# Kernel tuning notes

Measured on AMD Instinct MI355X. Metric: run time of the kernel, lower is better.

Reference implementation:

```python
import jax, jax.numpy as jnp
import numpy as np

HEADS = 8
DIM_HEAD = 64

def setup_inputs() -> dict:
    key = jax.random.key(0)
    ks = jax.random.split(key, 5)
    B, n, dim = 128, 512, 256
    inner = HEADS * DIM_HEAD  # 512
    return {
        'x': jax.random.normal(ks[0], (B, n, dim), dtype=jnp.float32),
        'Wq': jax.random.normal(ks[1], (dim, inner), dtype=jnp.float32) * (dim ** -0.5),
        'Wkv': jax.random.normal(ks[2], (dim, 2 * inner), dtype=jnp.float32) * (dim ** -0.5),
        'Wo': jax.random.normal(ks[3], (inner, dim), dtype=jnp.float32) * (inner ** -0.5),
        'bo': jnp.zeros((dim,), dtype=jnp.float32),
        'tie_attn_dim': 64,
    }

def reference(x, Wq, Wkv, Wo, bo, tie_attn_dim):
    h, dh = HEADS, DIM_HEAD
    B, n, dim = x.shape
    r = tie_attn_dim
    b = B // r
    q = x @ Wq                      # [B, n, h*dh]
    kv = x @ Wkv                    # [B, n, 2*h*dh] (self-attention: context = x)
    k, v = jnp.split(kv, 2, axis=-1)
    # '(b r) n (h d) -> b r h n d'
    def to_tied(t):
        return t.reshape(b, r, n, h, dh).transpose(0, 1, 3, 2, 4)
    q, k, v = map(to_tied, (q, k, v))
    scale = (dh ** -0.5) * (r ** -0.5)
    # tied row attention: reduce over MSA rows r and head dim d
    dots = jnp.einsum('brhid,brhjd->bhij', q, k) * scale  # [b, h, n, n]
    attn = jax.nn.softmax(dots, axis=-1)
    out = jnp.einsum('bhij,brhjd->brhid', attn, v)        # [b, r, h, n, dh]
    # 'b r h n d -> (b r) n (h d)'
    out = out.transpose(0, 1, 3, 2, 4).reshape(B, n, h * dh)
    return out @ Wo + bo
```

## Files before the change

kernel.cpp:

```cpp
#include <hip/hip_runtime.h>

typedef unsigned short u16;
typedef __attribute__((ext_vector_type(8))) short bf16x8;
typedef __attribute__((ext_vector_type(4))) float f32x4;

struct __align__(8) U16x4 { u16 a, b, c, d; };

__device__ __forceinline__ u16 f2bf(float f) {
  union { float f; unsigned int u; } cv; cv.f = f;
  unsigned int u = cv.u;
  unsigned int r = (u + 0x7fffu + ((u >> 16) & 1u)) >> 16;
  return (u16)r;
}

__device__ __forceinline__ void gld16(const u16* g, u16* l) {
  __builtin_amdgcn_global_load_lds((const __attribute__((address_space(1))) void*)g,
                                   (__attribute__((address_space(3))) void*)l, 16, 0, 0);
}

__global__ void conv_k(const float* __restrict__ x, u16* __restrict__ xbf) {
  size_t i = ((size_t)blockIdx.x * 256 + threadIdx.x) * 8;
  u16 tmp[8];
  #pragma unroll
  for (int j = 0; j < 8; j++) tmp[j] = f2bf(x[i + j]);
  *(bf16x8*)&xbf[i] = *(const bf16x8*)&tmp[0];
}

__global__ void prep_k(const float* __restrict__ Wq, const float* __restrict__ Wkv,
                       const float* __restrict__ Wo, u16* __restrict__ WT1,
                       u16* __restrict__ WoT) {
  int idx = blockIdx.x * 256 + threadIdx.x;
  if (idx < 1536 * 256) {
    int c = idx >> 8, k = idx & 255;
    WT1[idx] = (c < 512) ? f2bf(Wq[(size_t)k * 512 + c])
                         : f2bf(Wkv[(size_t)k * 1024 + (c - 512)]);
  }
  if (idx < 256 * 512) {
    int nn = idx >> 9, kk = idx & 511;
    WoT[idx] = f2bf(Wo[(size_t)kk * 256 + nn]);
  }
}

template<int KIND>
__global__ void __launch_bounds__(256, 3) gemm_k(
    const u16* __restrict__ A, const u16* __restrict__ B,
    u16* __restrict__ C, u16* __restrict__ C2,
    float* __restrict__ SF, const float* __restrict__ bias,
    int aux0, int nk32) {
  __shared__ __align__(16) u16 lsm[16384];
  u16* lAq[2] = { lsm,        lsm + 4096 };
  u16* lBq[2] = { lsm + 8192, lsm + 12288 };

  const int tid  = threadIdx.x;
  const int bid  = blockIdx.x;
  const int lane = tid & 63;
  const int wv   = tid >> 6;
  const int l15  = lane & 15;
  const int quad = lane >> 4;
  const int mq   = (wv & 1) * 64;
  const int nq   = (wv >> 1) * 64;

  int m0, n0, NK2, kb0 = 0;
  int s = 0, p = 0;
  if constexpr (KIND == 1) {
    int nwg = aux0 * 12;
    int per = nwg >> 3;
    int sw  = (bid & 7) * per + (bid >> 3);
    m0 = (sw / 12) * 128; n0 = (sw % 12) * 128; NK2 = 4;
  } else if constexpr (KIND == 2) {
    int npS = aux0;
    n0 = (bid & 3) * 128; m0 = ((bid >> 2) & 3) * 128;
    p = (bid >> 4) & ((1 << npS) - 1); s = bid >> (4 + npS);
    NK2 = nk32 >> 1; kb0 = s * nk32;
  } else if constexpr (KIND == 3) {
    n0 = (bid & 31) * 128; m0 = ((bid >> 5) & 3) * 128; p = bid >> 7; NK2 = 8;
  } else {
    n0 = (bid & 1) * 128; m0 = (bid >> 1) * 128; NK2 = 8;
  }

  f32x4 acc[4][4];
  #pragma unroll
  for (int i = 0; i < 4; i++)
    #pragma unroll
    for (int j = 0; j < 4; j++)
      #pragma unroll
      for (int g = 0; g < 4; g++) acc[i][j][g] = 0.f;

  const int ar0 = tid >> 2;
  const int ac0 = (tid & 3) * 8;

  for (int t = 0; t < NK2; t++) {
    #pragma unroll
    for (int q = 0; q < 2; q++) {
      const int kb = kb0 + 2 * t + q;
      size_t aBase, bBase; int aRS, bRS;
      if constexpr (KIND == 1) {
        aBase = (size_t)m0 * 256 + kb * 32; aRS = 256;
        bBase = (size_t)n0 * 256 + kb * 32; bRS = 256;
      } else if constexpr (KIND == 2) {
        int bt = p >> 3, hl = p & 7;
        int r = kb >> 1, dlo = (kb & 1) * 32;
        size_t rowblk = (size_t)bt * 32768 + (size_t)r * 512;
        aBase = (rowblk + m0) * 1024 + hl * 64 + dlo;        aRS = 1024;
        bBase = (rowblk + n0) * 1024 + 512 + hl * 64 + dlo;  bRS = 1024;
      } else if constexpr (KIND == 3) {
        aBase = ((size_t)p * 512 + m0) * 512 + kb * 32;   aRS = 512;
        bBase = ((size_t)p * 4096 + n0) * 512 + kb * 32;  bRS = 512;
      } else {
        int bt = m0 >> 15, h = kb >> 1, dlo = (kb & 1) * 32;
        aBase = ((size_t)(bt * 8 + h) * 512 + (m0 & 511)) * 4096
                + ((m0 >> 9) & 63) * 64 + dlo;
        aRS = 4096;
        bBase = (size_t)n0 * 512 + kb * 32; bRS = 512;
      }
      gld16(A + aBase + (size_t)ar0 * aRS + ac0,        &lAq[q][tid * 8]);
      gld16(A + aBase + (size_t)(ar0 + 64) * aRS + ac0, &lAq[q][(tid + 256) * 8]);
      gld16(B + bBase + (size_t)ar0 * bRS + ac0,        &lBq[q][tid * 8]);
      gld16(B + bBase + (size_t)(ar0 + 64) * bRS + ac0, &lBq[q][(tid + 256) * 8]);
    }
    __syncthreads();

    #pragma unroll
    for (int q = 0; q < 2; q++) {
      bf16x8 af[4], bfr[4];
      #pragma unroll
      for (int mi = 0; mi < 4; mi++)
        af[mi] = *(const bf16x8*)&lAq[q][(mq + mi * 16 + l15) * 32 + quad * 8];
      #pragma unroll
      for (int ni = 0; ni < 4; ni++)
        bfr[ni] = *(const bf16x8*)&lBq[q][(nq + ni * 16 + l15) * 32 + quad * 8];
      #pragma unroll
      for (int mi = 0; mi < 4; mi++)
        #pragma unroll
        for (int ni = 0; ni < 4; ni++)
          acc[mi][ni] = __builtin_amdgcn_mfma_f32_16x16x32_bf16(af[mi], bfr[ni], acc[mi][ni], 0, 0, 0);
    }
    __syncthreads();
  }

  if constexpr (KIND == 1 || KIND == 3) {
    if (KIND == 3 || n0 < 1024) {
      #pragma unroll
      for (int ps = 0; ps < 2; ps++) {
        if ((mq >> 6) == ps) {
          #pragma unroll
          for (int mi = 0; mi < 4; mi++)
            #pragma unroll
            for (int ni = 0; ni < 4; ni++) {
              int lr = mi * 16 + quad * 4;
              int lc = nq + ni * 16 + l15;
              #pragma unroll
              for (int g = 0; g < 4; g++)
                lsm[(lr + g) * 136 + lc] = f2bf(acc[mi][ni][g]);
            }
        }
        __syncthreads();
        #pragma unroll
        for (int it = 0; it < 4; it++) {
          int idx = tid + it * 256;
          int lr = idx >> 4, c = (idx & 15) * 8;
          int gm = m0 + ps * 64 + lr;
          size_t gaddr;
          if constexpr (KIND == 1) gaddr = (size_t)gm * 1024 + n0 + c;
          else                     gaddr = ((size_t)p * 512 + gm) * 4096 + n0 + c;
          *(bf16x8*)&C[gaddr] = *(const bf16x8*)&lsm[lr * 136 + c];
        }
        __syncthreads();
      }
    } else {
      #pragma unroll
      for (int ps = 0; ps < 2; ps++) {
        if ((nq >> 6) == ps) {
          #pragma unroll
          for (int mi = 0; mi < 4; mi++)
            #pragma unroll
            for (int ni = 0; ni < 4; ni++) {
              int lrn = ni * 16 + l15;
              int lcm = mq + mi * 16 + quad * 4;
              U16x4 pk;
              pk.a = f2bf(acc[mi][ni][0]); pk.b = f2bf(acc[mi][ni][1]);
              pk.c = f2bf(acc[mi][ni][2]); pk.d = f2bf(acc[mi][ni][3]);
              *(U16x4*)&lsm[lrn * 136 + lcm] = pk;
            }
        }
        __syncthreads();
        int bt2 = m0 >> 15;
        int r  = (m0 >> 9) & 63;
        int jb = (m0 & 511);
        #pragma unroll
        for (int it = 0; it < 4; it++) {
          int idx = tid + it * 256;
          int lr = idx >> 4, c = (idx & 15) * 8;
          int cc = (n0 - 1024) + ps * 64 + lr;
          int h = cc >> 6, d = cc & 63;
          size_t gaddr = ((size_t)(bt2 * 8 + h) * 4096 + r * 64 + d) * 512 + jb + c;
          *(bf16x8*)&C2[gaddr] = *(const bf16x8*)&lsm[lr * 136 + c];
        }
        __syncthreads();
      }
    }
  } else {
    float* lsf = (float*)lsm;
    #pragma unroll
    for (int ps = 0; ps < 4; ps++) {
      if ((mq >> 6) == (ps >> 1)) {
        int miA = (ps & 1) * 2;
        #pragma unroll
        for (int mm = 0; mm < 2; mm++) {
          int mi = miA + mm;
          #pragma unroll
          for (int ni = 0; ni < 4; ni++) {
            int lr = mm * 16 + quad * 4;
            int lc = nq + ni * 16 + l15;
            #pragma unroll
            for (int g = 0; g < 4; g++)
              lsf[(lr + g) * 132 + lc] = acc[mi][ni][g];
          }
        }
      }
      __syncthreads();
      #pragma unroll
      for (int it = 0; it < 4; it++) {
        int idx = tid + it * 256;
        int lr = idx >> 5, c = (idx & 31) * 4;
        int gm = m0 + ps * 32 + lr;
        f32x4 v = *(const f32x4*)&lsf[lr * 132 + c];
        if constexpr (KIND == 2) {
          int npS = aux0;
          *(f32x4*)&SF[((size_t)((s << npS) + p) * 512 + gm) * 512 + n0 + c] = v;
        } else {
          f32x4 bo4 = *(const f32x4*)&bias[n0 + c];
          v[0] += bo4[0]; v[1] += bo4[1]; v[2] += bo4[2]; v[3] += bo4[3];
          *(f32x4*)&SF[(size_t)gm * 256 + n0 + c] = v;
        }
      }
      __syncthreads();
    }
  }
}

__global__ void softmax_k(const float* __restrict__ SP, u16* __restrict__ P,
                          int nsplit, int np) {
  int bid = blockIdx.x;
  int p = bid >> 9, i = bid & 511;
  int t = threadIdx.x;
  size_t rowbase = ((size_t)p * 512 + i) * 512;
  float v0 = 0.f, v1 = 0.f;
  for (int ss = 0; ss < nsplit; ss++) {
    size_t off = (size_t)ss * np * 512 * 512;
    v0 += SP[off + rowbase + t];
    v1 += SP[off + rowbase + t + 256];
  }
  const float scale = 1.0f / 64.0f;
  v0 *= scale; v1 *= scale;

  int wv = t >> 6, ln = t & 63;
  float m = fmaxf(v0, v1);
  for (int o = 32; o > 0; o >>= 1) m = fmaxf(m, __shfl_down(m, o));
  __shared__ float sred[4];
  if (ln == 0) sred[wv] = m;
  __syncthreads();
  m = fmaxf(fmaxf(sred[0], sred[1]), fmaxf(sred[2], sred[3]));

  float e0 = expf(v0 - m), e1 = expf(v1 - m);
  float sum = e0 + e1;
  for (int o = 32; o > 0; o >>= 1) sum += __shfl_down(sum, o);
  __shared__ float sred2[4];
  if (ln == 0) sred2[wv] = sum;
  __syncthreads();
  float inv = 1.0f / (sred2[0] + sred2[1] + sred2[2] + sred2[3]);

  P[rowbase + t]       = f2bf(e0 * inv);
  P[rowbase + t + 256] = f2bf(e1 * inv);
}

extern "C" void kernel_launch(void* const* d_in, const int* in_sizes, int n_in,
                              void* d_out, int out_size, void* d_ws, size_t ws_size,
                              hipStream_t stream) {
  (void)in_sizes; (void)n_in; (void)out_size;
  const float* x   = (const float*)d_in[0];
  const float* Wq  = (const float*)d_in[1];
  const float* Wkv = (const float*)d_in[2];
  const float* Wo  = (const float*)d_in[3];
  const float* bo  = (const float*)d_in[4];
  float* out = (float*)d_out;

  const size_t MB = 1024ull * 1024ull;
  int nsplit_m = (ws_size >= 266 * MB) ? 4 : 2;
  bool merged = (ws_size >= 202 * MB + ((nsplit_m * 16 * MB > 33 * MB)
                                         ? nsplit_m * 16 * MB : 33 * MB));

  char* ws = (char*)d_ws;
  size_t off = 0;
  u16* WT1 = (u16*)(ws + off); off += (size_t)1536 * 256 * 2;
  u16* WoT = (u16*)(ws + off); off += (size_t)256 * 512 * 2;

  prep_k<<<dim3(1536), dim3(256), 0, stream>>>(Wq, Wkv, Wo, WT1, WoT);

  if (merged) {
    const int np = 16, npS = 4, ns = nsplit_m;
    u16* QK = (u16*)(ws + off); off += (size_t)65536 * 1024 * 2;
    u16* OT = QK;
    u16* VT = (u16*)(ws + off); off += (size_t)np * 4096 * 512 * 2;
    u16* Pb = (u16*)(ws + off); off += (size_t)np * 512 * 512 * 2;
    char* XS = ws + off;
    u16* xbf = (u16*)XS;
    float* SP = (float*)XS;

    conv_k<<<dim3(8192), dim3(256), 0, stream>>>(x, xbf);
    gemm_k<1><<<dim3(512 * 12), dim3(256), 0, stream>>>(xbf, WT1, QK, VT,
                                                        nullptr, nullptr, 512, 0);
    gemm_k<2><<<dim3(ns * np * 16), dim3(256), 0, stream>>>(QK, QK, nullptr, nullptr,
                                                            SP, nullptr, npS, 128 / ns);
    softmax_k<<<dim3(np * 512), dim3(256), 0, stream>>>(SP, Pb, ns, np);
    gemm_k<3><<<dim3(np * 128), dim3(256), 0, stream>>>(Pb, VT, OT, nullptr,
                                                        nullptr, nullptr, 0, 0);
    gemm_k<4><<<dim3(1024), dim3(256), 0, stream>>>(OT, WoT, nullptr, nullptr,
                                                    out, bo, 0, 0);
  } else {
    const int np = 8, npS = 3;
    u16* QKb = (u16*)(ws + off); off += (size_t)32768 * 1024 * 2;
    u16* OTb = QKb;
    u16* VTb = (u16*)(ws + off); off += (size_t)np * 4096 * 512 * 2;
    u16* Pb  = (u16*)(ws + off); off += (size_t)np * 512 * 512 * 2;
    char* XS = ws + off;
    u16* xbf = (u16*)XS;
    float* SPb = (float*)XS;
    size_t rem = (ws_size > off) ? (ws_size - off) : 0;
    int ns = 4;
    while (ns > 1 && (size_t)ns * np * 512 * 512 * 4 > rem) ns >>= 1;

    for (int bt = 0; bt < 2; bt++) {
      const float* xb = x + (size_t)bt * 32768 * 256;
      float* outb = out + (size_t)bt * 32768 * 256;
      conv_k<<<dim3(4096), dim3(256), 0, stream>>>(xb, xbf);
      gemm_k<1><<<dim3(256 * 12), dim3(256), 0, stream>>>(xbf, WT1, QKb, VTb,
                                                          nullptr, nullptr, 256, 0);
      gemm_k<2><<<dim3(ns * np * 16), dim3(256), 0, stream>>>(QKb, QKb, nullptr, nullptr,
                                                              SPb, nullptr, npS, 128 / ns);
      softmax_k<<<dim3(np * 512), dim3(256), 0, stream>>>(SPb, Pb, ns, np);
      gemm_k<3><<<dim3(np * 128), dim3(256), 0, stream>>>(Pb, VTb, OTb, nullptr,
                                                          nullptr, nullptr, 0, 0);
      gemm_k<4><<<dim3(512), dim3(256), 0, stream>>>(OTb, WoT, nullptr, nullptr,
                                                     outb, bo, 0, 0);
    }
  }
}
```

Before: 358.0 us.

## Fuse fp32-to-bf16 conversion of x into projection GEMM loads

Removes the separate conv_k pass and has the QKV projection GEMM read fp32 x directly, converting to bf16 in registers before writing to LDS, which drops one full read and write of x. The softmax kernel now loads float2 and stores packed bf16 pairs, which changes the column-to-thread mapping but stays consistent. The split count for the scores GEMM is fixed at 2 and the workspace threshold for the merged path is changed. In exchange the A operand of the first GEMM loses the async global-to-LDS load and goes through registers with synchronous loads, and it needs twice the bytes per element.

```diff
diff --git a/kernel.cpp b/kernel.cpp
--- a/kernel.cpp
+++ b/kernel.cpp
@@ -16,14 +16,6 @@
 __device__ __forceinline__ void gld16(const u16* g, u16* l) {
   __builtin_amdgcn_global_load_lds((const __attribute__((address_space(1))) void*)g,
                                    (__attribute__((address_space(3))) void*)l, 16, 0, 0);
-}
-
-__global__ void conv_k(const float* __restrict__ x, u16* __restrict__ xbf) {
-  size_t i = ((size_t)blockIdx.x * 256 + threadIdx.x) * 8;
-  u16 tmp[8];
-  #pragma unroll
-  for (int j = 0; j < 8; j++) tmp[j] = f2bf(x[i + j]);
-  *(bf16x8*)&xbf[i] = *(const bf16x8*)&tmp[0];
 }
 
 __global__ void prep_k(const float* __restrict__ Wq, const float* __restrict__ Wkv,
@@ -93,30 +85,48 @@
     #pragma unroll
     for (int q = 0; q < 2; q++) {
       const int kb = kb0 + 2 * t + q;
-      size_t aBase, bBase; int aRS, bRS;
       if constexpr (KIND == 1) {
-        aBase = (size_t)m0 * 256 + kb * 32; aRS = 256;
-        bBase = (size_t)n0 * 256 + kb * 32; bRS = 256;
-      } else if constexpr (KIND == 2) {
-        int bt = p >> 3, hl = p & 7;
-        int r = kb >> 1, dlo = (kb & 1) * 32;
-        size_t rowblk = (size_t)bt * 32768 + (size_t)r * 512;
-        aBase = (rowblk + m0) * 1024 + hl * 64 + dlo;        aRS = 1024;
-        bBase = (rowblk + n0) * 1024 + 512 + hl * 64 + dlo;  bRS = 1024;
-      } else if constexpr (KIND == 3) {
-        aBase = ((size_t)p * 512 + m0) * 512 + kb * 32;   aRS = 512;
-        bBase = ((size_t)p * 4096 + n0) * 512 + kb * 32;  bRS = 512;
+        const float* xf = (const float*)A;
+        const float* pa = xf + (size_t)m0 * 256 + (size_t)kb * 32
+                             + (size_t)ar0 * 256 + ac0;
+        f32x4 u0 = *(const f32x4*)pa;
+        f32x4 u1 = *(const f32x4*)(pa + 4);
+        f32x4 u2 = *(const f32x4*)(pa + 64 * 256);
+        f32x4 u3 = *(const f32x4*)(pa + 64 * 256 + 4);
+        u16 c0[8], c1[8];
+        #pragma unroll
+        for (int j = 0; j < 4; j++) {
+          c0[j] = f2bf(u0[j]); c0[j + 4] = f2bf(u1[j]);
+          c1[j] = f2bf(u2[j]); c1[j + 4] = f2bf(u3[j]);
+        }
+        *(bf16x8*)&lAq[q][tid * 8]         = *(const bf16x8*)&c0[0];
+        *(bf16x8*)&lAq[q][(tid + 256) * 8] = *(const bf16x8*)&c1[0];
+        size_t bBase = (size_t)n0 * 256 + kb * 32;
+        gld16(B + bBase + (size_t)ar0 * 256 + ac0,        &lBq[q][tid * 8]);
+        gld16(B + bBase + (size_t)(ar0 + 64) * 256 + ac0, &lBq[q][(tid + 256) * 8]);
       } else {
-        int bt = m0 >> 15, h = kb >> 1, dlo = (kb & 1) * 32;
-        aBase = ((size_t)(bt * 8 + h) * 512 + (m0 & 511)) * 4096
-                + ((m0 >> 9) & 63) * 64 + dlo;
-        aRS = 4096;
-        bBase = (size_t)n0 * 512 + kb * 32; bRS = 512;
-      }
-      gld16(A + aBase + (size_t)ar0 * aRS + ac0,        &lAq[q][tid * 8]);
-      gld16(A + aBase + (size_t)(ar0 + 64) * aRS + ac0, &lAq[q][(tid + 256) * 8]);
-      gld16(B + bBase + (size_t)ar0 * bRS + ac0,        &lBq[q][tid * 8]);
-      gld16(B + bBase + (size_t)(ar0 + 64) * bRS + ac0, &lBq[q][(tid + 256) * 8]);
+        size_t aBase, bBase; int aRS, bRS;
+        if constexpr (KIND == 2) {
+          int bt = p >> 3, hl = p & 7;
+          int r = kb >> 1, dlo = (kb & 1) * 32;
+          size_t rowblk = (size_t)bt * 32768 + (size_t)r * 512;
+          aBase = (rowblk + m0) * 1024 + hl * 64 + dlo;        aRS = 1024;
+          bBase = (rowblk + n0) * 1024 + 512 + hl * 64 + dlo;  bRS = 1024;
+        } else if constexpr (KIND == 3) {
+          aBase = ((size_t)p * 512 + m0) * 512 + kb * 32;   aRS = 512;
+          bBase = ((size_t)p * 4096 + n0) * 512 + kb * 32;  bRS = 512;
+        } else {
+          int bt = m0 >> 15, h = kb >> 1, dlo = (kb & 1) * 32;
+          aBase = ((size_t)(bt * 8 + h) * 512 + (m0 & 511)) * 4096
+                  + ((m0 >> 9) & 63) * 64 + dlo;
+          aRS = 4096;
+          bBase = (size_t)n0 * 512 + kb * 32; bRS = 512;
+        }
+        gld16(A + aBase + (size_t)ar0 * aRS + ac0,        &lAq[q][tid * 8]);
+        gld16(A + aBase + (size_t)(ar0 + 64) * aRS + ac0, &lAq[q][(tid + 256) * 8]);
+        gld16(B + bBase + (size_t)ar0 * bRS + ac0,        &lBq[q][tid * 8]);
+        gld16(B + bBase + (size_t)(ar0 + 64) * bRS + ac0, &lBq[q][(tid + 256) * 8]);
+      }
     }
     __syncthreads();
 
@@ -248,8 +258,8 @@
   float v0 = 0.f, v1 = 0.f;
   for (int ss = 0; ss < nsplit; ss++) {
     size_t off = (size_t)ss * np * 512 * 512;
-    v0 += SP[off + rowbase + t];
-    v1 += SP[off + rowbase + t + 256];
+    float2 u = *(const float2*)&SP[off + rowbase + 2 * t];
+    v0 += u.x; v1 += u.y;
   }
   const float scale = 1.0f / 64.0f;
   v0 *= scale; v1 *= scale;
@@ -270,8 +280,9 @@
   __syncthreads();
   float inv = 1.0f / (sred2[0] + sred2[1] + sred2[2] + sred2[3]);
 
-  P[rowbase + t]       = f2bf(e0 * inv);
-  P[rowbase + t + 256] = f2bf(e1 * inv);
+  unsigned int pk = (unsigned int)f2bf(e0 * inv)
+                  | ((unsigned int)f2bf(e1 * inv) << 16);
+  *(unsigned int*)&P[rowbase + 2 * t] = pk;
 }
 
 extern "C" void kernel_launch(void* const* d_in, const int* in_sizes, int n_in,
@@ -286,9 +297,8 @@
   float* out = (float*)d_out;
 
   const size_t MB = 1024ull * 1024ull;
-  int nsplit_m = (ws_size >= 266 * MB) ? 4 : 2;
-  bool merged = (ws_size >= 202 * MB + ((nsplit_m * 16 * MB > 33 * MB)
-                                         ? nsplit_m * 16 * MB : 33 * MB));
+  const int ns_m = 2;
+  bool merged = (ws_size >= 240 * MB);
 
   char* ws = (char*)d_ws;
   size_t off = 0;
@@ -298,17 +308,14 @@
   prep_k<<<dim3(1536), dim3(256), 0, stream>>>(Wq, Wkv, Wo, WT1, WoT);
 
   if (merged) {
-    const int np = 16, npS = 4, ns = nsplit_m;
+    const int np = 16, npS = 4, ns = ns_m;
     u16* QK = (u16*)(ws + off); off += (size_t)65536 * 1024 * 2;
     u16* OT = QK;
     u16* VT = (u16*)(ws + off); off += (size_t)np * 4096 * 512 * 2;
     u16* Pb = (u16*)(ws + off); off += (size_t)np * 512 * 512 * 2;
-    char* XS = ws + off;
-    u16* xbf = (u16*)XS;
-    float* SP = (float*)XS;
-
-    conv_k<<<dim3(8192), dim3(256), 0, stream>>>(x, xbf);
-    gemm_k<1><<<dim3(512 * 12), dim3(256), 0, stream>>>(xbf, WT1, QK, VT,
+    float* SP = (float*)(ws + off);
+
+    gemm_k<1><<<dim3(512 * 12), dim3(256), 0, stream>>>((const u16*)x, WT1, QK, VT,
                                                         nullptr, nullptr, 512, 0);
     gemm_k<2><<<dim3(ns * np * 16), dim3(256), 0, stream>>>(QK, QK, nullptr, nullptr,
                                                             SP, nullptr, npS, 128 / ns);
@@ -323,18 +330,15 @@
     u16* OTb = QKb;
     u16* VTb = (u16*)(ws + off); off += (size_t)np * 4096 * 512 * 2;
     u16* Pb  = (u16*)(ws + off); off += (size_t)np * 512 * 512 * 2;
-    char* XS = ws + off;
-    u16* xbf = (u16*)XS;
-    float* SPb = (float*)XS;
+    float* SPb = (float*)(ws + off);
     size_t rem = (ws_size > off) ? (ws_size - off) : 0;
-    int ns = 4;
+    int ns = 2;
     while (ns > 1 && (size_t)ns * np * 512 * 512 * 4 > rem) ns >>= 1;
 
     for (int bt = 0; bt < 2; bt++) {
       const float* xb = x + (size_t)bt * 32768 * 256;
       float* outb = out + (size_t)bt * 32768 * 256;
-      conv_k<<<dim3(4096), dim3(256), 0, stream>>>(xb, xbf);
-      gemm_k<1><<<dim3(256 * 12), dim3(256), 0, stream>>>(xbf, WT1, QKb, VTb,
+      gemm_k<1><<<dim3(256 * 12), dim3(256), 0, stream>>>((const u16*)xb, WT1, QKb, VTb,
                                                           nullptr, nullptr, 256, 0);
       gemm_k<2><<<dim3(ns * np * 16), dim3(256), 0, stream>>>(QKb, QKb, nullptr, nullptr,
                                                               SPb, nullptr, npS, 128 / ns);
```

Measured after the change: 414.4 us. 15.7% more time.
